# Performance work log

Hardware: AMD Instinct MI355X
Metric: run time of the kernel (lower is better)

The kernel has to match this reference:

```python
import jax, jax.numpy as jnp
import numpy as np
import math

B, T, D, H = 4, 2048, 1024, 16
DH = D // H

def setup_inputs() -> dict:
    key = jax.random.key(0)
    ks = jax.random.split(key, 12)
    s = 1.0 / math.sqrt(D)
    inp = {
        'q': jax.random.normal(ks[0], (B, T, D), jnp.float32),
        'k': jax.random.normal(ks[1], (B, T, D), jnp.float32),
        'v': jax.random.normal(ks[2], (B, T, D), jnp.float32),
        # causal attn_mask [B, Tq, Tk]; all-keep padding mask [B,1,1,Tk]
        'attn_mask': jnp.broadcast_to(jnp.tril(jnp.ones((T, T), jnp.bool_)), (B, T, T)),
        'key_keep_mask': jnp.ones((B, 1, 1, T), jnp.bool_),
        'wq_w': jax.random.normal(ks[3], (D, D), jnp.float32) * s,
        'wq_b': jnp.zeros((D,), jnp.float32),
        'wk_w': jax.random.normal(ks[4], (D, D), jnp.float32) * s,
        'wk_b': jnp.zeros((D,), jnp.float32),
        'wv_w': jax.random.normal(ks[5], (D, D), jnp.float32) * s,
        'wv_b': jnp.zeros((D,), jnp.float32),
        'wo_w': jax.random.normal(ks[6], (D, D), jnp.float32) * s,
        'wo_b': jnp.zeros((D,), jnp.float32),
    }
    return inp

def reference(q, k, v, attn_mask, key_keep_mask, wq_w, wq_b, wk_w, wk_b, wv_w, wv_b, wo_w, wo_b):
    # projections (torch Linear: x @ W^T + b)
    Q = (q @ wq_w.T + wq_b).reshape(B, -1, H, DH).transpose(0, 2, 1, 3)  # [B,H,Tq,DH]
    K = (k @ wk_w.T + wk_b).reshape(B, -1, H, DH).transpose(0, 2, 1, 3)
    V = (v @ wv_w.T + wv_b).reshape(B, -1, H, DH).transpose(0, 2, 1, 3)
    scores = jnp.einsum('bhqd,bhkd->bhqk', Q, K) / math.sqrt(DH)
    neg_inf = jnp.array(-jnp.inf, scores.dtype)
    scores = jnp.where(attn_mask[:, None, :, :], scores, neg_inf)
    scores = jnp.where(key_keep_mask, scores, neg_inf)
    attn = jax.nn.softmax(scores, axis=-1)  # dropout p=0 -> identity
    out = jnp.einsum('bhqk,bhkd->bhqd', attn, V)
    out = out.transpose(0, 2, 1, 3).reshape(B, -1, D)
    return out @ wo_w.T + wo_b
```

## Files before the change

kernel.cpp:

```cpp
#include <hip/hip_runtime.h>
#include <cstdint>
#include <cstddef>


typedef float f32x4 __attribute__((ext_vector_type(4)));
typedef short bf16x8 __attribute__((ext_vector_type(8)));
typedef float fltx4 __attribute__((ext_vector_type(4)));
typedef unsigned short u16x4 __attribute__((ext_vector_type(4)));

#define GLOBAL_AS __attribute__((address_space(1)))
#define LDS_AS __attribute__((address_space(3)))

__device__ __forceinline__ unsigned short f2bf(float f) {
    union { float f; unsigned int u; } x;
    x.f = f;
    unsigned int u = x.u;
    unsigned int r = (u + 0x7FFFu + ((u >> 16) & 1u)) >> 16;
    return (unsigned short)r;
}

__device__ __forceinline__ unsigned int cvtpk_bf16(float lo, float hi) {
    unsigned int d;
    asm("v_cvt_pk_bf16_f32 %0, %1, %2" : "=v"(d) : "v"(lo), "v"(hi));
    return d;
}

__device__ __forceinline__ unsigned int pack_trunc(float a, float b) {
    union { float f; unsigned int u; } x, y;
    x.f = a; y.f = b;
    return (x.u >> 16) | (y.u & 0xFFFF0000u);
}

__global__ __launch_bounds__(256) void wcast_kernel(
    const float* __restrict__ wq, const float* __restrict__ wk,
    const float* __restrict__ wv, const float* __restrict__ wo,
    unsigned short* __restrict__ dst)
{
    const size_t WSEG = 1048576;
    size_t i = ((size_t)blockIdx.x * 256 + threadIdx.x) * 4;
    const float* src;
    size_t off;
    if (i < WSEG)          { src = wq; off = i; }
    else if (i < 2 * WSEG) { src = wk; off = i - WSEG; }
    else if (i < 3 * WSEG) { src = wv; off = i - 2 * WSEG; }
    else                   { src = wo; off = i - 3 * WSEG; }
    fltx4 val = *(const fltx4*)(src + off);
    u16x4 o;
    o[0] = f2bf(val[0]);
    o[1] = f2bf(val[1]);
    o[2] = f2bf(val[2]);
    o[3] = f2bf(val[3]);
    *(u16x4*)(dst + i) = o;
}

__global__ __launch_bounds__(256, 3) void qkv_gemm_kernel(
    const float* __restrict__ q, const float* __restrict__ k,
    const float* __restrict__ v,
    const unsigned short* __restrict__ Wc,
    const float* __restrict__ bq, const float* __restrict__ bk,
    const float* __restrict__ bv,
    unsigned short* __restrict__ Outs,
    float qscale)
{
    const int z = blockIdx.y;
    const float* A = (z == 0) ? q : (z == 1) ? k : v;
    const unsigned short* Bw = Wc + (size_t)z * 1048576;
    const float* bias = (z == 0) ? bq : (z == 1) ? bk : bv;
    unsigned short* outp = Outs + (size_t)z * 8388608;
    const float scale = (z == 0) ? qscale : 1.0f;
    const bool vmode = (z == 2);

    __shared__ __align__(16) unsigned short lds[3 * 8192];

    const int tid = threadIdx.x;
    const int w = tid >> 6, lane = tid & 63;
    const int quad = lane >> 4, l16 = lane & 15;
    const int wr = w >> 1, wc = w & 1;

    const int lin = blockIdx.x;
    const int r_ = lin & 7, s_ = lin >> 3;
    const int bm = ((r_ << 3) | (s_ & 7)) * 128;
    const int bn = (s_ >> 3) * 128;

    const int rq = lane >> 2;
    const int cq = lane & 3;
    const int arow0 = w * 32;

    fltx4 areg[2][2];

    auto issueA = [&](int kt) {
#pragma unroll
        for (int s = 0; s < 2; ++s) {
            const float* p = A + (size_t)(bm + arow0 + s * 16 + rq) * 1024 + kt * 32 + cq * 8;
            areg[s][0] = *(const fltx4*)p;
            areg[s][1] = *(const fltx4*)(p + 4);
        }
    };
    auto writeA = [&](int buf) {
        unsigned short* lA = lds + buf * 8192;
#pragma unroll
        for (int s = 0; s < 2; ++s) {
            int row = arow0 + s * 16 + rq;
            int chunk = cq ^ ((row >> 1) & 3);
            uint4 pk;
            pk.x = cvtpk_bf16(areg[s][0][0], areg[s][0][1]);
            pk.y = cvtpk_bf16(areg[s][0][2], areg[s][0][3]);
            pk.z = cvtpk_bf16(areg[s][1][0], areg[s][1][1]);
            pk.w = cvtpk_bf16(areg[s][1][2], areg[s][1][3]);
            *(uint4*)(lA + row * 32 + chunk * 8) = pk;
        }
    };
    auto issueB = [&](int kt, int buf) {
        unsigned short* lB = lds + buf * 8192 + 4096;
#pragma unroll
        for (int g = 0; g < 2; ++g) {
            int r0 = w * 32 + g * 16;
            int row = r0 + rq;
            int csw = cq ^ ((row >> 1) & 3);
            __builtin_amdgcn_global_load_lds(
                (const GLOBAL_AS unsigned int*)(Bw + (size_t)(bn + row) * 1024 + kt * 32 + csw * 8),
                (LDS_AS unsigned int*)(lB + r0 * 32), 16, 0, 0);
        }
    };

    f32x4 acc[4][4] = {};

    issueA(0); issueB(0, 0);
    asm volatile("s_waitcnt vmcnt(2)" ::: "memory");
    writeA(0);
    issueA(1); issueB(1, 1);

    for (int kt = 0; kt < 32; ++kt) {
        const int cur = kt % 3;
        if (kt < 31) {
            asm volatile("s_waitcnt vmcnt(2)" ::: "memory");
            writeA((kt + 1) % 3);
        } else {
            asm volatile("s_waitcnt vmcnt(0)" ::: "memory");
        }
        asm volatile("s_waitcnt lgkmcnt(0)" ::: "memory");
        __builtin_amdgcn_sched_barrier(0);
        __builtin_amdgcn_s_barrier();
        __builtin_amdgcn_sched_barrier(0);
        if (kt < 30) { issueA(kt + 2); issueB(kt + 2, (kt + 2) % 3); }

        const unsigned short* lA = lds + cur * 8192;
        const unsigned short* lB = lA + 4096;
        bf16x8 af[4], bfr[4];
#pragma unroll
        for (int mi = 0; mi < 4; ++mi) {
            int row = wr * 64 + mi * 16 + l16;
            af[mi] = *(const bf16x8*)(lA + row * 32 + ((quad ^ ((row >> 1) & 3)) * 8));
        }
#pragma unroll
        for (int ni = 0; ni < 4; ++ni) {
            int row = wc * 64 + ni * 16 + l16;
            bfr[ni] = *(const bf16x8*)(lB + row * 32 + ((quad ^ ((row >> 1) & 3)) * 8));
        }
        __builtin_amdgcn_s_setprio(1);
#pragma unroll
        for (int mi = 0; mi < 4; ++mi)
#pragma unroll
            for (int ni = 0; ni < 4; ++ni)
                acc[mi][ni] = __builtin_amdgcn_mfma_f32_16x16x32_bf16(
                    af[mi], bfr[ni], acc[mi][ni], 0, 0, 0);
        __builtin_amdgcn_s_setprio(0);
    }

#pragma unroll
    for (int mi = 0; mi < 4; ++mi) {
        int rowb = bm + wr * 64 + mi * 16 + quad * 4;
#pragma unroll
        for (int ni = 0; ni < 4; ++ni) {
            int col = bn + wc * 64 + ni * 16 + l16;
            float bv_ = bias[col];
            if (!vmode) {
#pragma unroll
                for (int r = 0; r < 4; ++r) {
                    int m = rowb + r;
                    float vout = (acc[mi][ni][r] + bv_) * scale;
                    int b = m >> 11, t = m & 2047, h = col >> 6, d = col & 63;
                    outp[((size_t)(b * 16 + h) * 2048 + t) * 64 + d] = f2bf(vout);
                }
            } else {
                u16x4 o;
#pragma unroll
                for (int r = 0; r < 4; ++r)
                    o[r] = f2bf(acc[mi][ni][r] + bv_);
                int b = rowb >> 11, t0 = rowb & 2047, h = col >> 6, d = col & 63;
                *(u16x4*)(outp + ((size_t)(b * 16 + h) * 64 + d) * 2048 + t0) = o;
            }
        }
    }
}

__global__ __launch_bounds__(256, 3) void out_gemm_kernel(
    const unsigned short* __restrict__ A,
    const unsigned short* __restrict__ Bw,
    const float* __restrict__ bias,
    float* __restrict__ outp)
{
    __shared__ __align__(16) unsigned short lds[3 * 8192];

    const int tid = threadIdx.x;
    const int w = tid >> 6, lane = tid & 63;
    const int quad = lane >> 4, l16 = lane & 15;
    const int wr = w >> 1, wc = w & 1;

    const int lin = blockIdx.x;
    const int r_ = lin & 7, s_ = lin >> 3;
    const int bm = ((r_ << 3) | (s_ & 7)) * 128;
    const int bn = (s_ >> 3) * 128;

    const int rq = lane >> 2;
    const int cq = lane & 3;

    auto stage = [&](int kt, int buf) {
        unsigned short* lA = lds + buf * 8192;
        unsigned short* lB = lA + 4096;
#pragma unroll
        for (int g = 0; g < 2; ++g) {
            int r0 = w * 32 + g * 16;
            int row = r0 + rq;
            int csw = cq ^ ((row >> 1) & 3);
            __builtin_amdgcn_global_load_lds(
                (const GLOBAL_AS unsigned int*)(A + (size_t)(bm + row) * 1024 + kt * 32 + csw * 8),
                (LDS_AS unsigned int*)(lA + r0 * 32), 16, 0, 0);
            __builtin_amdgcn_global_load_lds(
                (const GLOBAL_AS unsigned int*)(Bw + (size_t)(bn + row) * 1024 + kt * 32 + csw * 8),
                (LDS_AS unsigned int*)(lB + r0 * 32), 16, 0, 0);
        }
    };

    f32x4 acc[4][4] = {};

    stage(0, 0);
    stage(1, 1);

    for (int kt = 0; kt < 32; ++kt) {
        const int cur = kt % 3;
        if (kt < 31) asm volatile("s_waitcnt vmcnt(4)" ::: "memory");
        else         asm volatile("s_waitcnt vmcnt(0)" ::: "memory");
        __builtin_amdgcn_sched_barrier(0);
        __builtin_amdgcn_s_barrier();
        __builtin_amdgcn_sched_barrier(0);
        if (kt < 30) stage(kt + 2, (kt + 2) % 3);

        const unsigned short* lA = lds + cur * 8192;
        const unsigned short* lB = lA + 4096;
        bf16x8 af[4], bfr[4];
#pragma unroll
        for (int mi = 0; mi < 4; ++mi) {
            int row = wr * 64 + mi * 16 + l16;
            af[mi] = *(const bf16x8*)(lA + row * 32 + ((quad ^ ((row >> 1) & 3)) * 8));
        }
#pragma unroll
        for (int ni = 0; ni < 4; ++ni) {
            int row = wc * 64 + ni * 16 + l16;
            bfr[ni] = *(const bf16x8*)(lB + row * 32 + ((quad ^ ((row >> 1) & 3)) * 8));
        }
        __builtin_amdgcn_s_setprio(1);
#pragma unroll
        for (int mi = 0; mi < 4; ++mi)
#pragma unroll
            for (int ni = 0; ni < 4; ++ni)
                acc[mi][ni] = __builtin_amdgcn_mfma_f32_16x16x32_bf16(
                    af[mi], bfr[ni], acc[mi][ni], 0, 0, 0);
        __builtin_amdgcn_s_setprio(0);
    }

#pragma unroll
    for (int mi = 0; mi < 4; ++mi) {
        int rowb = bm + wr * 64 + mi * 16 + quad * 4;
#pragma unroll
        for (int ni = 0; ni < 4; ++ni) {
            int col = bn + wc * 64 + ni * 16 + l16;
            float bv_ = bias[col];
#pragma unroll
            for (int r = 0; r < 4; ++r)
                outp[(size_t)(rowb + r) * 1024 + col] = acc[mi][ni][r] + bv_;
        }
    }
}

__global__ __launch_bounds__(256) void attn_kernel(
    const unsigned short* __restrict__ Qh,
    const unsigned short* __restrict__ Kh,
    const unsigned short* __restrict__ Vt,
    unsigned short* __restrict__ att)
{
    const int tid = threadIdx.x;
    const int w = tid >> 6, lane = tid & 63;
    const int qd = lane >> 4, l16 = lane & 15;
    const int bh = blockIdx.x;
    const int pairy = blockIdx.y;

    const unsigned short* Qp = Qh + (size_t)bh * 2048 * 64;
    const unsigned short* Kp = Kh + (size_t)bh * 2048 * 64;
    const unsigned short* Vp = Vt + (size_t)bh * 64 * 2048;
    const int b = bh >> 4, h = bh & 15;

    __shared__ __align__(16) unsigned short Kl[3][64 * 64];
    __shared__ __align__(16) unsigned short Vl[3][64 * 64];
    __shared__ __align__(16) unsigned short Pl[4][2][16 * 64];

    auto stage = [&](int kt, int buf) {
#pragma unroll
        for (int j = 0; j < 2; ++j) {
            int r = w * 16 + j * 8 + (lane >> 3);
            int c = (lane & 7) ^ (r & 7);
            __builtin_amdgcn_global_load_lds(
                (const GLOBAL_AS unsigned int*)(Kp + (size_t)(kt * 64 + r) * 64 + c * 8),
                (LDS_AS unsigned int*)(&Kl[buf][(w * 16 + j * 8) * 64]), 16, 0, 0);
            __builtin_amdgcn_global_load_lds(
                (const GLOBAL_AS unsigned int*)(Vp + (size_t)r * 2048 + kt * 64 + c * 8),
                (LDS_AS unsigned int*)(&Vl[buf][(w * 16 + j * 8) * 64]), 16, 0, 0);
        }
    };

    auto run_phase = [&](int qblk) {
        const int wqbase = qblk * 128 + w * 32;
        const int ktmax = 2 * qblk + 1;

        bf16x8 qa[2][2];
#pragma unroll
        for (int qt = 0; qt < 2; ++qt)
#pragma unroll
            for (int ks = 0; ks < 2; ++ks)
                qa[qt][ks] = *(const bf16x8*)(Qp + (size_t)(wqbase + qt * 16 + l16) * 64 + ks * 32 + qd * 8);

        float lp[2] = {0.0f, 0.0f};
        f32x4 O[2][4] = {};

        __builtin_amdgcn_s_barrier();
        stage(0, 0);
        stage(1, 1);

        for (int kt = 0; kt <= ktmax; ++kt) {
            if (kt < ktmax) asm volatile("s_waitcnt vmcnt(4)" ::: "memory");
            else            asm volatile("s_waitcnt vmcnt(0)" ::: "memory");
            __builtin_amdgcn_s_barrier();
            if (kt + 2 <= ktmax) stage(kt + 2, (kt + 2) % 3);

            if (kt * 64 <= wqbase + 31) {
                const unsigned short* kl = &Kl[kt % 3][0];
                const unsigned short* vl = &Vl[kt % 3][0];

                bf16x8 kf[4][2];
#pragma unroll
                for (int nt = 0; nt < 4; ++nt)
#pragma unroll
                    for (int ks = 0; ks < 2; ++ks)
                        kf[nt][ks] = *(const bf16x8*)(kl + (nt * 16 + l16) * 64 +
                                                      (((ks * 4 + qd) ^ (l16 & 7)) * 8));

                f32x4 S[2][4];
#pragma unroll
                for (int qt = 0; qt < 2; ++qt)
#pragma unroll
                    for (int nt = 0; nt < 4; ++nt) {
                        f32x4 a = {};
                        a = __builtin_amdgcn_mfma_f32_16x16x32_bf16(kf[nt][0], qa[qt][0], a, 0, 0, 0);
                        a = __builtin_amdgcn_mfma_f32_16x16x32_bf16(kf[nt][1], qa[qt][1], a, 0, 0, 0);
                        S[qt][nt] = a;
                    }

                if (kt * 64 + 63 > wqbase) {
#pragma unroll
                    for (int qt = 0; qt < 2; ++qt) {
                        int qrow = wqbase + qt * 16 + l16;
#pragma unroll
                        for (int nt = 0; nt < 4; ++nt) {
                            int kbase = kt * 64 + nt * 16 + qd * 4;
#pragma unroll
                            for (int r = 0; r < 4; ++r)
                                if (kbase + r > qrow) S[qt][nt][r] = -INFINITY;
                        }
                    }
                }

#pragma unroll
                for (int qt = 0; qt < 2; ++qt) {
                    float s0 = 0.0f;
#pragma unroll
                    for (int nt = 0; nt < 4; ++nt)
#pragma unroll
                        for (int r = 0; r < 4; ++r) {
                            float e = __builtin_amdgcn_exp2f(S[qt][nt][r]);
                            S[qt][nt][r] = e;
                            s0 += e;
                        }
                    lp[qt] += s0;
                }

#pragma unroll
                for (int qt = 0; qt < 2; ++qt) {
                    unsigned short* pw = &Pl[w][qt][0];
#pragma unroll
                    for (int nt = 0; nt < 4; ++nt) {
                        uint2 pv;
                        pv.x = pack_trunc(S[qt][nt][0], S[qt][nt][1]);
                        pv.y = pack_trunc(S[qt][nt][2], S[qt][nt][3]);
                        int chunk = (2 * nt + (qd >> 1)) ^ (l16 & 7);
                        *(uint2*)(pw + l16 * 64 + chunk * 8 + (qd & 1) * 4) = pv;
                    }
                }
                asm volatile("s_waitcnt lgkmcnt(0)" ::: "memory");

                bf16x8 pa[2][2];
#pragma unroll
                for (int qt = 0; qt < 2; ++qt)
#pragma unroll
                    for (int s = 0; s < 2; ++s)
                        pa[qt][s] = *(const bf16x8*)(&Pl[w][qt][0] + l16 * 64 +
                                                     (((s * 4 + qd) ^ (l16 & 7)) * 8));

                bf16x8 vf[2][4];
#pragma unroll
                for (int s = 0; s < 2; ++s)
#pragma unroll
                    for (int dh = 0; dh < 4; ++dh)
                        vf[s][dh] = *(const bf16x8*)(vl + (dh * 16 + l16) * 64 +
                                                     (((s * 4 + qd) ^ (l16 & 7)) * 8));
#pragma unroll
                for (int qt = 0; qt < 2; ++qt)
#pragma unroll
                    for (int dh = 0; dh < 4; ++dh) {
                        O[qt][dh] = __builtin_amdgcn_mfma_f32_16x16x32_bf16(pa[qt][0], vf[0][dh], O[qt][dh], 0, 0, 0);
                        O[qt][dh] = __builtin_amdgcn_mfma_f32_16x16x32_bf16(pa[qt][1], vf[1][dh], O[qt][dh], 0, 0, 0);
                    }
            }
        }

#pragma unroll
        for (int qt = 0; qt < 2; ++qt) {
            float lsum = lp[qt];
            lsum += __shfl_xor(lsum, 16, 64);
            lsum += __shfl_xor(lsum, 32, 64);
            float linv = 1.0f / lsum;
#pragma unroll
            for (int r = 0; r < 4; ++r) {
                float lC = __shfl(linv, qd * 4 + r, 64);
                int t = wqbase + qt * 16 + qd * 4 + r;
#pragma unroll
                for (int dh = 0; dh < 4; ++dh) {
                    size_t idx = (size_t)(b * 2048 + t) * 1024 + h * 64 + dh * 16 + l16;
                    att[idx] = f2bf(O[qt][dh][r] * lC);
                }
            }
        }
    };

    run_phase(15 - pairy);
    run_phase(pairy);
}

extern "C" void kernel_launch(void* const* d_in, const int* in_sizes, int n_in,
                              void* d_out, int out_size, void* d_ws, size_t ws_size,
                              hipStream_t stream)
{
    const float* q = (const float*)d_in[0];
    const float* k = (const float*)d_in[1];
    const float* v = (const float*)d_in[2];
    const float* wq_w = (const float*)d_in[5];
    const float* wq_b = (const float*)d_in[6];
    const float* wk_w = (const float*)d_in[7];
    const float* wk_b = (const float*)d_in[8];
    const float* wv_w = (const float*)d_in[9];
    const float* wv_b = (const float*)d_in[10];
    const float* wo_w = (const float*)d_in[11];
    const float* wo_b = (const float*)d_in[12];

    unsigned short* ws = (unsigned short*)d_ws;
    unsigned short* xq  = ws;
    unsigned short* wqc = ws + 25165824;
    unsigned short* woc = ws + 28311552;
    unsigned short* Qhp = ws + 29360128;
    unsigned short* Khp = ws + 37748736;
    unsigned short* Vtp = ws + 46137344;
    unsigned short* att = xq;

    (void)in_sizes; (void)n_in; (void)out_size; (void)ws_size;

    wcast_kernel<<<4096, 256, 0, stream>>>(wq_w, wk_w, wv_w, wo_w, wqc);

    qkv_gemm_kernel<<<dim3(512, 3), 256, 0, stream>>>(
        q, k, v, wqc, wq_b, wk_b, wv_b, Qhp, 0.1803368801f);

    attn_kernel<<<dim3(64, 8), 256, 0, stream>>>(Qhp, Khp, Vtp, att);

    out_gemm_kernel<<<512, 256, 0, stream>>>(att, woc, wo_b, (float*)d_out);
}
```

Measured before the change: 348.3 us.

## Enlarge QKV GEMM tile to 128x256 with 512-thread blocks

The QKV projection GEMM moves from 128x128 tiles with 4 waves to 128x256 tiles with 8 waves, halving the grid and increasing reuse of the fp32 A tile, which is converted to bf16 once per block. The A-operand staging is reorganised so each wave loads one 16-row slice, and the LDS write for the next stage now happens after the barrier instead of before it. This cuts redundant global reads of the fp32 activations at the cost of more LDS per block and fewer blocks for load balance. The block swizzle is rewritten to the new tile shape.

```diff
diff --git a/kernel.cpp b/kernel.cpp
--- a/kernel.cpp
+++ b/kernel.cpp
@@ -53,7 +53,7 @@
     *(u16x4*)(dst + i) = o;
 }
 
-__global__ __launch_bounds__(256, 3) void qkv_gemm_kernel(
+__global__ __launch_bounds__(512, 2) void qkv_gemm_kernel(
     const float* __restrict__ q, const float* __restrict__ k,
     const float* __restrict__ v,
     const unsigned short* __restrict__ Wc,
@@ -70,48 +70,39 @@
     const float scale = (z == 0) ? qscale : 1.0f;
     const bool vmode = (z == 2);
 
-    __shared__ __align__(16) unsigned short lds[3 * 8192];
+    __shared__ __align__(16) unsigned short lds[3 * 12288];
 
     const int tid = threadIdx.x;
     const int w = tid >> 6, lane = tid & 63;
     const int quad = lane >> 4, l16 = lane & 15;
-    const int wr = w >> 1, wc = w & 1;
+    const int wr = w >> 2, wn = w & 3;
 
     const int lin = blockIdx.x;
     const int r_ = lin & 7, s_ = lin >> 3;
-    const int bm = ((r_ << 3) | (s_ & 7)) * 128;
-    const int bn = (s_ >> 3) * 128;
+    const int bm = (r_ * 8 + (s_ >> 4) * 4 + (s_ & 3)) * 128;
+    const int bn = ((s_ >> 2) & 3) * 256;
 
     const int rq = lane >> 2;
     const int cq = lane & 3;
-    const int arow0 = w * 32;
-
-    fltx4 areg[2][2];
-
-    auto issueA = [&](int kt) {
-#pragma unroll
-        for (int s = 0; s < 2; ++s) {
-            const float* p = A + (size_t)(bm + arow0 + s * 16 + rq) * 1024 + kt * 32 + cq * 8;
-            areg[s][0] = *(const fltx4*)p;
-            areg[s][1] = *(const fltx4*)(p + 4);
-        }
-    };
-    auto writeA = [&](int buf) {
-        unsigned short* lA = lds + buf * 8192;
-#pragma unroll
-        for (int s = 0; s < 2; ++s) {
-            int row = arow0 + s * 16 + rq;
-            int chunk = cq ^ ((row >> 1) & 3);
-            uint4 pk;
-            pk.x = cvtpk_bf16(areg[s][0][0], areg[s][0][1]);
-            pk.y = cvtpk_bf16(areg[s][0][2], areg[s][0][3]);
-            pk.z = cvtpk_bf16(areg[s][1][0], areg[s][1][1]);
-            pk.w = cvtpk_bf16(areg[s][1][2], areg[s][1][3]);
-            *(uint4*)(lA + row * 32 + chunk * 8) = pk;
-        }
+    const int arow = w * 16 + rq;
+    const float* Abase = A + (size_t)(bm + arow) * 1024 + cq * 8;
+    const int asl = arow * 32 + ((cq ^ ((arow >> 1) & 3)) * 8);
+
+    fltx4 a0, a1;
+
+    auto ldA = [&](int kt) {
+        const float* p = Abase + kt * 32;
+        a0 = *(const fltx4*)p;
+        a1 = *(const fltx4*)(p + 4);
+    };
+    auto wrA = [&](int buf) {
+        uint4 pk;
+        pk.x = cvtpk_bf16(a0[0], a0[1]); pk.y = cvtpk_bf16(a0[2], a0[3]);
+        pk.z = cvtpk_bf16(a1[0], a1[1]); pk.w = cvtpk_bf16(a1[2], a1[3]);
+        *(uint4*)(lds + buf * 12288 + asl) = pk;
     };
     auto issueB = [&](int kt, int buf) {
-        unsigned short* lB = lds + buf * 8192 + 4096;
+        unsigned short* lB = lds + buf * 12288 + 4096;
 #pragma unroll
         for (int g = 0; g < 2; ++g) {
             int r0 = w * 32 + g * 16;
@@ -125,26 +116,26 @@
 
     f32x4 acc[4][4] = {};
 
-    issueA(0); issueB(0, 0);
-    asm volatile("s_waitcnt vmcnt(2)" ::: "memory");
-    writeA(0);
-    issueA(1); issueB(1, 1);
+    ldA(0);
+    asm volatile("s_waitcnt vmcnt(0)" ::: "memory");
+    wrA(0);
+    issueB(0, 0);
+    ldA(1);
+    issueB(1, 1);
+    asm volatile("s_waitcnt lgkmcnt(0)" ::: "memory");
 
     for (int kt = 0; kt < 32; ++kt) {
         const int cur = kt % 3;
-        if (kt < 31) {
-            asm volatile("s_waitcnt vmcnt(2)" ::: "memory");
-            writeA((kt + 1) % 3);
-        } else {
-            asm volatile("s_waitcnt vmcnt(0)" ::: "memory");
-        }
-        asm volatile("s_waitcnt lgkmcnt(0)" ::: "memory");
+        if (kt < 31) asm volatile("s_waitcnt vmcnt(2)" ::: "memory");
+        else         asm volatile("s_waitcnt vmcnt(0)" ::: "memory");
         __builtin_amdgcn_sched_barrier(0);
         __builtin_amdgcn_s_barrier();
         __builtin_amdgcn_sched_barrier(0);
-        if (kt < 30) { issueA(kt + 2); issueB(kt + 2, (kt + 2) % 3); }
-
-        const unsigned short* lA = lds + cur * 8192;
+
+        if (kt < 31) wrA((kt + 1) % 3);
+        if (kt < 30) { ldA(kt + 2); issueB(kt + 2, (kt + 2) % 3); }
+
+        const unsigned short* lA = lds + cur * 12288;
         const unsigned short* lB = lA + 4096;
         bf16x8 af[4], bfr[4];
 #pragma unroll
@@ -154,7 +145,7 @@
         }
 #pragma unroll
         for (int ni = 0; ni < 4; ++ni) {
-            int row = wc * 64 + ni * 16 + l16;
+            int row = wn * 64 + ni * 16 + l16;
             bfr[ni] = *(const bf16x8*)(lB + row * 32 + ((quad ^ ((row >> 1) & 3)) * 8));
         }
         __builtin_amdgcn_s_setprio(1);
@@ -172,7 +163,7 @@
         int rowb = bm + wr * 64 + mi * 16 + quad * 4;
 #pragma unroll
         for (int ni = 0; ni < 4; ++ni) {
-            int col = bn + wc * 64 + ni * 16 + l16;
+            int col = bn + wn * 64 + ni * 16 + l16;
             float bv_ = bias[col];
             if (!vmode) {
 #pragma unroll
@@ -484,7 +475,7 @@
 
     wcast_kernel<<<4096, 256, 0, stream>>>(wq_w, wk_w, wv_w, wo_w, wqc);
 
-    qkv_gemm_kernel<<<dim3(512, 3), 256, 0, stream>>>(
+    qkv_gemm_kernel<<<dim3(256, 3), 512, 0, stream>>>(
         q, k, v, wqc, wq_b, wk_b, wv_b, Qhp, 0.1803368801f);
 
     attn_kernel<<<dim3(64, 8), 256, 0, stream>>>(Qhp, Khp, Vtp, att);
```

Result: slower. 357.5 us (+2.6%).
